# Performance work log

Hardware: AMD Instinct MI355X
Metric: run time of the kernel (lower is better)

The kernel has to match this reference:

```python
import jax, jax.numpy as jnp
import numpy as np

N = 50000      # num nodes
E = 800000     # num edges
D = 128        # num_hid
EPS = 1e-8


def _mlp(x, w1, b1, w2, b2):
    # 2-layer MLP: Linear -> ReLU -> Linear (dropout disabled at inference)
    return jax.nn.relu(x @ w1 + b1) @ w2 + b2


def setup_inputs() -> dict:
    key = jax.random.key(0)
    ks = jax.random.split(key, 12)

    def lin(k, fan_in, fan_out):
        kw, kb = jax.random.split(k)
        lim = 1.0 / np.sqrt(fan_in)
        w = jax.random.uniform(kw, (fan_in, fan_out), jnp.float32, -lim, lim)
        b = jax.random.uniform(kb, (fan_out,), jnp.float32, -lim, lim)
        return w, b

    H = jax.random.normal(ks[0], (N, D), jnp.float32)
    edge_index = jax.random.randint(ks[1], (2, E), 0, N, jnp.int64)
    w1_1, b1_1 = lin(ks[2], 2 * D, D)   # mlp_1 layer 1
    w1_2, b1_2 = lin(ks[3], D, D)       # mlp_1 layer 2
    w2_1, b2_1 = lin(ks[4], 2 * D, D)   # mlp_2 layer 1
    w2_2, b2_2 = lin(ks[5], D, 1)       # mlp_2 layer 2 (channel_curv=False -> out=1)
    t = jnp.zeros((), jnp.float32)
    return {"t": t, "H": H, "edge_index": edge_index,
            "w1_1": w1_1, "b1_1": b1_1, "w1_2": w1_2, "b1_2": b1_2,
            "w2_1": w2_1, "b2_1": b2_1, "w2_2": w2_2, "b2_2": b2_2}


def reference(t, H, edge_index, w1_1, b1_1, w1_2, b1_2, w2_1, b2_1, w2_2, b2_2):
    src, dst = edge_index[0], edge_index[1]

    # damping: row-normalize H
    H = H / (jnp.linalg.norm(H, axis=1, keepdims=True) + EPS)

    H_i = H[src]                                    # [E, D]
    H_j = H[dst]                                    # [E, D]

    # curvature(H_i, H_j)
    c = jnp.concatenate((H_i, H_j), axis=1)         # [E, 2D]
    c = jax.nn.relu(_mlp(c, w1_1, b1_1, w1_2, b1_2))  # [E, D]
    c = jax.ops.segment_sum(c, src, num_segments=N)   # scatter-sum -> [N, D]
    c = jnp.concatenate((c[src], c[dst]), axis=1)     # [E, 2D]
    curv = _mlp(c, w2_1, b2_1, w2_2, b2_2)            # [E, 1]

    # damped edge message
    cos = jnp.sum(H_i * H_j, axis=1, keepdims=True)   # [E, 1]
    H_edge = curv * (H_j - cos * H_i)                 # [E, D]

    # scatter-mean over source node
    s = jax.ops.segment_sum(H_edge, src, num_segments=N)               # [N, D]
    cnt = jax.ops.segment_sum(jnp.ones((E, 1), H.dtype), src, num_segments=N)
    Hm = s / jnp.maximum(cnt, 1.0)

    # damping: row-normalize output
    return Hm / (jnp.linalg.norm(Hm, axis=1, keepdims=True) + EPS)
```

## Files before the change

kernel.cpp:

```cpp
#include <hip/hip_runtime.h>
#include <hip/hip_bf16.h>

#define D 128
#define EPS 1e-8f
#define E1S 136

typedef __attribute__((ext_vector_type(8))) short short8;
typedef __attribute__((ext_vector_type(4))) float f32x4;
typedef unsigned int uint;

__device__ inline short f2bf(float x) {
    union { float f; unsigned u; } v; v.f = x;
    unsigned u = v.u + 0x7fffu + ((v.u >> 16) & 1u);
    return (short)(u >> 16);
}
__device__ inline float b2f(short s) {
    union { unsigned u; float f; } v;
    v.u = ((unsigned)(unsigned short)s) << 16;
    return v.f;
}
__device__ inline float uasf(uint u) {
    union { unsigned u; float f; } v; v.u = u; return v.f;
}

__global__ void k_normalize(const float* __restrict__ H, short* __restrict__ Hnb, int N) {
    int row = blockIdx.x * 4 + (threadIdx.x >> 6);
    int lane = threadIdx.x & 63;
    if (row >= N) return;
    float2 v = reinterpret_cast<const float2*>(H + (size_t)row * D)[lane];
    float ss = v.x * v.x + v.y * v.y;
    #pragma unroll
    for (int off = 32; off; off >>= 1) ss += __shfl_xor(ss, off, 64);
    float scale = 1.0f / (sqrtf(ss) + EPS);
    uint p = ((uint)(unsigned short)f2bf(v.x * scale)) |
             (((uint)(unsigned short)f2bf(v.y * scale)) << 16);
    reinterpret_cast<uint*>(Hnb + (size_t)row * D)[lane] = p;
}

__global__ void k_hist(const int* __restrict__ src, int* __restrict__ deg, int E) {
    for (int e = blockIdx.x * blockDim.x + threadIdx.x; e < E; e += gridDim.x * blockDim.x)
        atomicAdd(&deg[src[e]], 1);
}

__global__ void k_scan(const int* __restrict__ deg, int* __restrict__ rowptr, int N) {
    __shared__ int wsum[16];
    __shared__ int carry;
    int t = threadIdx.x, lane = t & 63, w = t >> 6;
    if (t == 0) carry = 0;
    __syncthreads();
    for (int base = 0; base < N; base += 4096) {
        int i0 = base + t * 4;
        int a = 0, b = 0, c = 0, d = 0;
        if (i0 + 3 < N) {
            int4 v4 = *reinterpret_cast<const int4*>(deg + i0);
            a = v4.x; b = v4.y; c = v4.z; d = v4.w;
        } else {
            if (i0 < N) a = deg[i0];
            if (i0 + 1 < N) b = deg[i0 + 1];
            if (i0 + 2 < N) c = deg[i0 + 2];
            if (i0 + 3 < N) d = deg[i0 + 3];
        }
        int s1 = a + b, s2 = s1 + c, s3 = s2 + d;
        int v = s3;
        #pragma unroll
        for (int off = 1; off < 64; off <<= 1) {
            int u = __shfl_up(v, off, 64);
            if (lane >= off) v += u;
        }
        if (lane == 63) wsum[w] = v;
        __syncthreads();
        if (w == 0 && lane < 16) {
            int s = wsum[lane];
            #pragma unroll
            for (int off = 1; off < 16; off <<= 1) {
                int u = __shfl_up(s, off, 64);
                if (lane >= off) s += u;
            }
            wsum[lane] = s;
        }
        __syncthreads();
        int add = (w > 0 ? wsum[w - 1] : 0) + carry;
        int incl = v + add;
        int pre = incl - s3;
        if (i0 < N)     rowptr[i0 + 1] = pre + a;
        if (i0 + 1 < N) rowptr[i0 + 2] = pre + s1;
        if (i0 + 2 < N) rowptr[i0 + 3] = pre + s2;
        if (i0 + 3 < N) rowptr[i0 + 4] = pre + s3;
        __syncthreads();
        if (t == 1023) carry = incl;
        __syncthreads();
    }
    if (t == 0) rowptr[0] = 0;
}

__global__ void k_scatter(const int* __restrict__ src, const int* __restrict__ dst,
                          const int* __restrict__ rowptr, int* __restrict__ fill,
                          int* __restrict__ srcS, int* __restrict__ dstS, int E) {
    for (int e = blockIdx.x * blockDim.x + threadIdx.x; e < E; e += gridDim.x * blockDim.x) {
        int s = src[e];
        int pos = atomicAdd(&fill[s], 1);
        int idx = rowptr[s] + pos;
        srcS[idx] = s;
        dstS[idx] = dst[e];
    }
}

__global__ void k_prep_all(const float* __restrict__ w1_1, const float* __restrict__ w1_2,
                           const float* __restrict__ w2_1, short* __restrict__ Wt) {
    int b = blockIdx.x;
    int m = b >> 6;
    int idx = (b & 63) * 256 + threadIdx.x;
    int k = idx >> 7, n = idx & 127;
    const float* W = (m == 0) ? w1_1
                   : (m == 1) ? w1_1 + 16384
                   : (m == 2) ? w1_2
                   : (m == 3) ? w2_1
                              : w2_1 + 16384;
    Wt[m * 16384 + n * 128 + k] = f2bf(W[k * 128 + n]);
}

template <bool A_BF16>
__global__ __launch_bounds__(256, 4)
void k_gemm_dual(const void* __restrict__ Aptr, const short* __restrict__ Wt0,
                 const short* __restrict__ Wt1, const float* __restrict__ bias0,
                 short* __restrict__ out0, short* __restrict__ out1, int N) {
    __shared__ short As[64 * E1S];
    int t = threadIdx.x;
    int r0 = blockIdx.x * 64;
    int l = t & 63, w = t >> 6, n0 = w * 32;
    {
        int er = t >> 2, kb = (t & 3) * 32;
        int rc = min(r0 + er, N - 1);
        if (A_BF16) {
            const short8* Ap = reinterpret_cast<const short8*>((const short*)Aptr + (size_t)rc * 128 + kb);
            #pragma unroll
            for (int q = 0; q < 4; ++q)
                *reinterpret_cast<short8*>(&As[er * E1S + kb + q * 8]) = Ap[q];
        } else {
            const float4* Ap = reinterpret_cast<const float4*>((const float*)Aptr + (size_t)rc * 128 + kb);
            #pragma unroll
            for (int q = 0; q < 4; ++q) {
                float4 a0 = Ap[q * 2], a1 = Ap[q * 2 + 1];
                short8 sv;
                sv[0] = f2bf(a0.x); sv[1] = f2bf(a0.y); sv[2] = f2bf(a0.z); sv[3] = f2bf(a0.w);
                sv[4] = f2bf(a1.x); sv[5] = f2bf(a1.y); sv[6] = f2bf(a1.z); sv[7] = f2bf(a1.w);
                *reinterpret_cast<short8*>(&As[er * E1S + kb + q * 8]) = sv;
            }
        }
    }
    short8 bfrag[2][4];
    #pragma unroll
    for (int nt = 0; nt < 2; ++nt) {
        int col = n0 + nt * 16 + (l & 15);
        #pragma unroll
        for (int kt = 0; kt < 4; ++kt)
            bfrag[nt][kt] = *reinterpret_cast<const short8*>(Wt0 + col * 128 + kt * 32 + (l >> 4) * 8);
    }
    float b0a = bias0[n0 + (l & 15)];
    float b0b = bias0[n0 + 16 + (l & 15)];
    __syncthreads();
    f32x4 acc0[4][2], acc1[4][2];
    #pragma unroll
    for (int mt = 0; mt < 4; ++mt) {
        acc0[mt][0] = (f32x4){0,0,0,0}; acc0[mt][1] = (f32x4){0,0,0,0};
        acc1[mt][0] = (f32x4){0,0,0,0}; acc1[mt][1] = (f32x4){0,0,0,0};
    }
    #pragma unroll
    for (int mt = 0; mt < 4; ++mt) {
        int arow = mt * 16 + (l & 15);
        #pragma unroll
        for (int kt = 0; kt < 4; ++kt) {
            short8 af = *reinterpret_cast<const short8*>(&As[arow * E1S + kt * 32 + (l >> 4) * 8]);
            acc0[mt][0] = __builtin_amdgcn_mfma_f32_16x16x32_bf16(af, bfrag[0][kt], acc0[mt][0], 0, 0, 0);
            acc0[mt][1] = __builtin_amdgcn_mfma_f32_16x16x32_bf16(af, bfrag[1][kt], acc0[mt][1], 0, 0, 0);
        }
    }
    #pragma unroll
    for (int nt = 0; nt < 2; ++nt) {
        int col = n0 + nt * 16 + (l & 15);
        #pragma unroll
        for (int kt = 0; kt < 4; ++kt)
            bfrag[nt][kt] = *reinterpret_cast<const short8*>(Wt1 + col * 128 + kt * 32 + (l >> 4) * 8);
    }
    #pragma unroll
    for (int mt = 0; mt < 4; ++mt) {
        int arow = mt * 16 + (l & 15);
        #pragma unroll
        for (int kt = 0; kt < 4; ++kt) {
            short8 af = *reinterpret_cast<const short8*>(&As[arow * E1S + kt * 32 + (l >> 4) * 8]);
            acc1[mt][0] = __builtin_amdgcn_mfma_f32_16x16x32_bf16(af, bfrag[0][kt], acc1[mt][0], 0, 0, 0);
            acc1[mt][1] = __builtin_amdgcn_mfma_f32_16x16x32_bf16(af, bfrag[1][kt], acc1[mt][1], 0, 0, 0);
        }
    }
    __syncthreads();
    #pragma unroll
    for (int mt = 0; mt < 4; ++mt)
        #pragma unroll
        for (int j = 0; j < 4; ++j) {
            int row = mt * 16 + (l >> 4) * 4 + j;
            As[row * E1S + n0 + (l & 15)]      = f2bf(acc0[mt][0][j] + b0a);
            As[row * E1S + n0 + 16 + (l & 15)] = f2bf(acc0[mt][1][j] + b0b);
        }
    __syncthreads();
    {
        int er = t >> 2, kb = (t & 3) * 32;
        int row = r0 + er;
        if (row < N)
            #pragma unroll
            for (int q = 0; q < 4; ++q)
                *reinterpret_cast<short8*>(out0 + (size_t)row * 128 + kb + q * 8) =
                    *reinterpret_cast<const short8*>(&As[er * E1S + kb + q * 8]);
    }
    __syncthreads();
    #pragma unroll
    for (int mt = 0; mt < 4; ++mt)
        #pragma unroll
        for (int j = 0; j < 4; ++j) {
            int row = mt * 16 + (l >> 4) * 4 + j;
            As[row * E1S + n0 + (l & 15)]      = f2bf(acc1[mt][0][j]);
            As[row * E1S + n0 + 16 + (l & 15)] = f2bf(acc1[mt][1][j]);
        }
    __syncthreads();
    {
        int er = t >> 2, kb = (t & 3) * 32;
        int row = r0 + er;
        if (row < N)
            #pragma unroll
            for (int q = 0; q < 4; ++q)
                *reinterpret_cast<short8*>(out1 + (size_t)row * 128 + kb + q * 8) =
                    *reinterpret_cast<const short8*>(&As[er * E1S + kb + q * 8]);
    }
}

__global__ __launch_bounds__(256, 5)
void k_edge_mlp1(const int* __restrict__ srcS, const int* __restrict__ dstS,
                 const int* __restrict__ rowptr,
                 const short* __restrict__ P, const short* __restrict__ Q,
                 const short* __restrict__ Wt, const float* __restrict__ b1_2,
                 float* __restrict__ C, int E) {
    __shared__ short e1s[64 * E1S];
    int t = threadIdx.x;
    int e0 = blockIdx.x * 64;
    int l = t & 63, w = t >> 6, n0 = w * 32;
    {
        int er = t >> 2, kb = (t & 3) * 32;
        int ge = min(e0 + er, E - 1);
        int sc = srcS[ge], dj = dstS[ge];
        const short8* Pp = reinterpret_cast<const short8*>(P + (size_t)sc * 128 + kb);
        const short8* Qp = reinterpret_cast<const short8*>(Q + (size_t)dj * 128 + kb);
        #pragma unroll
        for (int q = 0; q < 4; ++q) {
            short8 pv = Pp[q], qv = Qp[q];
            short8 sv;
            #pragma unroll
            for (int i = 0; i < 8; ++i)
                sv[i] = f2bf(fmaxf(b2f(pv[i]) + b2f(qv[i]), 0.f));
            *reinterpret_cast<short8*>(&e1s[er * E1S + kb + q * 8]) = sv;
        }
    }
    short8 bfrag[2][4];
    #pragma unroll
    for (int nt = 0; nt < 2; ++nt) {
        int col = n0 + nt * 16 + (l & 15);
        #pragma unroll
        for (int kt = 0; kt < 4; ++kt)
            bfrag[nt][kt] = *reinterpret_cast<const short8*>(Wt + col * 128 + kt * 32 + (l >> 4) * 8);
    }
    float bias0 = b1_2[n0 + (l & 15)];
    float bias1 = b1_2[n0 + 16 + (l & 15)];
    __syncthreads();
    f32x4 acc[4][2];
    #pragma unroll
    for (int mt = 0; mt < 4; ++mt) { acc[mt][0] = (f32x4){0,0,0,0}; acc[mt][1] = (f32x4){0,0,0,0}; }
    #pragma unroll
    for (int mt = 0; mt < 4; ++mt) {
        int arow = mt * 16 + (l & 15);
        #pragma unroll
        for (int kt = 0; kt < 4; ++kt) {
            short8 af = *reinterpret_cast<const short8*>(&e1s[arow * E1S + kt * 32 + (l >> 4) * 8]);
            acc[mt][0] = __builtin_amdgcn_mfma_f32_16x16x32_bf16(af, bfrag[0][kt], acc[mt][0], 0, 0, 0);
            acc[mt][1] = __builtin_amdgcn_mfma_f32_16x16x32_bf16(af, bfrag[1][kt], acc[mt][1], 0, 0, 0);
        }
    }
    #pragma unroll
    for (int mt = 0; mt < 4; ++mt)
        #pragma unroll
        for (int j = 0; j < 4; ++j) {
            acc[mt][0][j] = fmaxf(acc[mt][0][j] + bias0, 0.f);
            acc[mt][1][j] = fmaxf(acc[mt][1][j] + bias1, 0.f);
        }
    int myv = (e0 + l < E) ? srcS[e0 + l] : -1;
    int pv = __shfl_up(myv, 1, 64);
    bool head = (l == 0) || (myv != pv);
    unsigned long long validm = __ballot(myv >= 0);
    unsigned long long hm = __ballot(head) & validm;
    int nvalid = __popcll(validm);
    int grp = l >> 4;
    while (hm) {
        int lo = __builtin_ctzll(hm);
        hm &= hm - 1;
        int hi = hm ? __builtin_ctzll(hm) : nvalid;
        int s = __shfl(myv, lo, 64);
        float v0 = 0.f, v1 = 0.f;
        #pragma unroll
        for (int mt = 0; mt < 4; ++mt)
            #pragma unroll
            for (int j = 0; j < 4; ++j) {
                int row = mt * 16 + grp * 4 + j;
                bool in = (row >= lo) && (row < hi);
                v0 += in ? acc[mt][0][j] : 0.f;
                v1 += in ? acc[mt][1][j] : 0.f;
            }
        v0 += __shfl_xor(v0, 16, 64); v0 += __shfl_xor(v0, 32, 64);
        v1 += __shfl_xor(v1, 16, 64); v1 += __shfl_xor(v1, 32, 64);
        if (l < 16) {
            int rs = rowptr[s], re = rowptr[s + 1];
            float* cp = C + (size_t)s * 128 + n0 + l;
            if (rs >= e0 && re <= e0 + 64) {
                cp[0] = v0; cp[16] = v1;
            } else {
                atomicAdd(cp, v0); atomicAdd(cp + 16, v1);
            }
        }
    }
}

__global__ void k_edge_scal(const int* __restrict__ srcS, const int* __restrict__ dstS,
                            const short* __restrict__ Hnb,
                            const short* __restrict__ Rb, const short* __restrict__ Tb,
                            const float* __restrict__ w2_2, const float* __restrict__ b2_2,
                            float2* __restrict__ CC, int E) {
    int t = threadIdx.x;
    int e = blockIdx.x * 16 + (t >> 4);
    int sl = t & 15;
    if (e >= E) return;
    int s = srcS[e], d = dstS[e];
    uint4 hiu = reinterpret_cast<const uint4*>(Hnb + (size_t)s * 128)[sl];
    uint4 hju = reinterpret_cast<const uint4*>(Hnb + (size_t)d * 128)[sl];
    uint4 rvu = reinterpret_cast<const uint4*>(Rb + (size_t)s * 128)[sl];
    uint4 tvu = reinterpret_cast<const uint4*>(Tb + (size_t)d * 128)[sl];
    float4 wv0 = reinterpret_cast<const float4*>(w2_2)[sl * 2];
    float4 wv1 = reinterpret_cast<const float4*>(w2_2)[sl * 2 + 1];
    const float* wvp = &wv0.x;
    float pcos = 0.f, pcur = 0.f;
    const uint* hip = &hiu.x;
    const uint* hjp = &hju.x;
    const uint* rvp = &rvu.x;
    const uint* tvp = &tvu.x;
    #pragma unroll
    for (int k = 0; k < 4; ++k) {
        float hix = uasf(hip[k] << 16), hiy = uasf(hip[k] & 0xffff0000u);
        float hjx = uasf(hjp[k] << 16), hjy = uasf(hjp[k] & 0xffff0000u);
        float rvx = uasf(rvp[k] << 16), rvy = uasf(rvp[k] & 0xffff0000u);
        float tvx = uasf(tvp[k] << 16), tvy = uasf(tvp[k] & 0xffff0000u);
        float w0 = (k < 2) ? ((k == 0) ? wv0.x : wv0.z) : ((k == 2) ? wv1.x : wv1.z);
        float w1 = (k < 2) ? ((k == 0) ? wv0.y : wv0.w) : ((k == 2) ? wv1.y : wv1.w);
        pcos += hix * hjx + hiy * hjy;
        pcur += fmaxf(rvx + tvx, 0.f) * w0 + fmaxf(rvy + tvy, 0.f) * w1;
    }
    (void)wvp;
    #pragma unroll
    for (int off = 1; off < 16; off <<= 1) {
        pcos += __shfl_xor(pcos, off, 64);
        pcur += __shfl_xor(pcur, off, 64);
    }
    if (sl == 0)
        CC[e] = make_float2(pcur + b2_2[0], pcos);
}

__global__ void k_node_curv(const int* __restrict__ dstS, const int* __restrict__ rowptr,
                            const short* __restrict__ Hnb, const float2* __restrict__ CC,
                            float* __restrict__ out, int N) {
    int node = blockIdx.x * 4 + (threadIdx.x >> 6);
    int lane = threadIdx.x & 63;
    if (node >= N) return;
    uint hiu = reinterpret_cast<const uint*>(Hnb + (size_t)node * 128)[lane];
    float hix = uasf(hiu << 16), hiy = uasf(hiu & 0xffff0000u);
    int lo = rowptr[node], hiE = rowptr[node + 1];
    float ax = 0.f, ay = 0.f, sc = 0.f;
    for (int e = lo; e < hiE; ++e) {
        int d = dstS[e];
        float2 cc = CC[e];
        uint hju = reinterpret_cast<const uint*>(Hnb + (size_t)d * 128)[lane];
        float hjx = uasf(hju << 16), hjy = uasf(hju & 0xffff0000u);
        ax += cc.x * hjx;
        ay += cc.x * hjy;
        sc += cc.x * cc.y;
    }
    float inv = 1.0f / fmaxf((float)(hiE - lo), 1.0f);
    ax = (ax - sc * hix) * inv;
    ay = (ay - sc * hiy) * inv;
    float ss = ax * ax + ay * ay;
    #pragma unroll
    for (int off = 32; off; off >>= 1) ss += __shfl_xor(ss, off, 64);
    float scale = 1.0f / (sqrtf(ss) + EPS);
    reinterpret_cast<float2*>(out + (size_t)node * 128)[lane] = make_float2(ax * scale, ay * scale);
}

extern "C" void kernel_launch(void* const* d_in, const int* in_sizes, int n_in,
                              void* d_out, int out_size, void* d_ws, size_t ws_size,
                              hipStream_t stream) {
    const float* H    = (const float*)d_in[1];
    const int*   ei   = (const int*)d_in[2];
    const float* w1_1 = (const float*)d_in[3];
    const float* b1_1 = (const float*)d_in[4];
    const float* w1_2 = (const float*)d_in[5];
    const float* b1_2 = (const float*)d_in[6];
    const float* w2_1 = (const float*)d_in[7];
    const float* b2_1 = (const float*)d_in[8];
    const float* w2_2 = (const float*)d_in[9];
    const float* b2_2 = (const float*)d_in[10];

    int N = in_sizes[1] / D;
    int E = in_sizes[2] / 2;
    const int* src = ei;
    const int* dst = ei + E;

    float* out = (float*)d_out;

    short* Hnb  = (short*)d_ws;
    short* Pb   = Hnb + (size_t)N * D;
    short* Qb   = Pb + (size_t)N * D;
    float* Cb   = (float*)(Qb + (size_t)N * D);
    float2* CC  = (float2*)(Cb + (size_t)N * D);
    short* Wt   = (short*)(CC + E);
    int* deg    = (int*)(Wt + 5 * 16384);
    int* rowptr = deg + N;
    int* fill   = rowptr + N + 1;
    int* srcS   = fill + N;
    int* dstS   = srcS + E;

    hipMemsetAsync(Cb, 0, (size_t)N * D * sizeof(float), stream);
    hipMemsetAsync(deg, 0, (3 * (size_t)N + 1) * sizeof(int), stream);

    k_normalize<<<(N + 3) / 4, 256, 0, stream>>>(H, Hnb, N);
    k_hist<<<1024, 256, 0, stream>>>(src, deg, E);
    k_scan<<<1, 1024, 0, stream>>>(deg, rowptr, N);
    k_scatter<<<1024, 256, 0, stream>>>(src, dst, rowptr, fill, srcS, dstS, E);
    k_prep_all<<<320, 256, 0, stream>>>(w1_1, w1_2, w2_1, Wt);

    k_gemm_dual<true><<<(N + 63) / 64, 256, 0, stream>>>(Hnb, Wt + 0 * 16384, Wt + 1 * 16384,
                                                         b1_1, Pb, Qb, N);
    k_edge_mlp1<<<(E + 63) / 64, 256, 0, stream>>>(srcS, dstS, rowptr, Pb, Qb,
                                                   Wt + 2 * 16384, b1_2, Cb, E);
    k_gemm_dual<false><<<(N + 63) / 64, 256, 0, stream>>>(Cb, Wt + 3 * 16384, Wt + 4 * 16384,
                                                          b2_1, Pb, Qb, N);
    k_edge_scal<<<(E + 15) / 16, 256, 0, stream>>>(srcS, dstS, Hnb, Pb, Qb, w2_2, b2_2, CC, E);
    k_node_curv<<<(N + 3) / 4, 256, 0, stream>>>(dstS, rowptr, Hnb, CC, out, N);
}
```

Baseline: 412.0 us.

## Switch intermediates to fp16 and fuse edge scalar kernel into node aggregation

Replaces bf16 storage and MFMA with fp16 throughout, which simplifies conversions and lets the edge_mlp1 relu-add be done with packed half arithmetic. It also removes the separate per-edge scalar kernel and its CC buffer, computing curvature and cosine inside the per-node CSR loop with full-wave reductions. This saves a launch and the E-sized intermediate round trip, and the source-side R row is loaded once per node. In exchange, each edge iteration in the node loop now runs two 6-step shuffle reductions serially, and fp16 has a narrower range than bf16.

Result: slower. 425.2 us (+3.2%).

```diff
diff --git a/kernel.cpp b/kernel.cpp
--- a/kernel.cpp
+++ b/kernel.cpp
@@ -5,25 +5,23 @@
 #define EPS 1e-8f
 #define E1S 136
 
-typedef __attribute__((ext_vector_type(8))) short short8;
+typedef _Float16 f16;
+typedef __attribute__((ext_vector_type(8))) _Float16 half8;
 typedef __attribute__((ext_vector_type(4))) float f32x4;
 typedef unsigned int uint;
 
-__device__ inline short f2bf(float x) {
-    union { float f; unsigned u; } v; v.f = x;
-    unsigned u = v.u + 0x7fffu + ((v.u >> 16) & 1u);
-    return (short)(u >> 16);
-}
-__device__ inline float b2f(short s) {
-    union { unsigned u; float f; } v;
-    v.u = ((unsigned)(unsigned short)s) << 16;
-    return v.f;
-}
-__device__ inline float uasf(uint u) {
-    union { unsigned u; float f; } v; v.u = u; return v.f;
-}
-
-__global__ void k_normalize(const float* __restrict__ H, short* __restrict__ Hnb, int N) {
+__device__ inline short f2h(float x) {
+    union { f16 h; short s; } v; v.h = (f16)x; return v.s;
+}
+__device__ inline float h2f(short s) {
+    union { short s; f16 h; } v; v.s = s; return (float)v.h;
+}
+__device__ inline float2 up2(uint u) {
+    union { uint u; f16 h[2]; } v; v.u = u;
+    return make_float2((float)v.h[0], (float)v.h[1]);
+}
+
+__global__ void k_normalize(const float* __restrict__ H, f16* __restrict__ Hn, int N) {
     int row = blockIdx.x * 4 + (threadIdx.x >> 6);
     int lane = threadIdx.x & 63;
     if (row >= N) return;
@@ -32,9 +30,10 @@
     #pragma unroll
     for (int off = 32; off; off >>= 1) ss += __shfl_xor(ss, off, 64);
     float scale = 1.0f / (sqrtf(ss) + EPS);
-    uint p = ((uint)(unsigned short)f2bf(v.x * scale)) |
-             (((uint)(unsigned short)f2bf(v.y * scale)) << 16);
-    reinterpret_cast<uint*>(Hnb + (size_t)row * D)[lane] = p;
+    union { f16 h[2]; uint u; } p;
+    p.h[0] = (f16)(v.x * scale);
+    p.h[1] = (f16)(v.y * scale);
+    reinterpret_cast<uint*>(Hn + (size_t)row * D)[lane] = p.u;
 }
 
 __global__ void k_hist(const int* __restrict__ src, int* __restrict__ deg, int E) {
@@ -106,7 +105,7 @@
 }
 
 __global__ void k_prep_all(const float* __restrict__ w1_1, const float* __restrict__ w1_2,
-                           const float* __restrict__ w2_1, short* __restrict__ Wt) {
+                           const float* __restrict__ w2_1, f16* __restrict__ Wt) {
     int b = blockIdx.x;
     int m = b >> 6;
     int idx = (b & 63) * 256 + threadIdx.x;
@@ -116,45 +115,45 @@
                    : (m == 2) ? w1_2
                    : (m == 3) ? w2_1
                               : w2_1 + 16384;
-    Wt[m * 16384 + n * 128 + k] = f2bf(W[k * 128 + n]);
-}
-
-template <bool A_BF16>
+    Wt[m * 16384 + n * 128 + k] = (f16)W[k * 128 + n];
+}
+
+template <bool A_F16>
 __global__ __launch_bounds__(256, 4)
-void k_gemm_dual(const void* __restrict__ Aptr, const short* __restrict__ Wt0,
-                 const short* __restrict__ Wt1, const float* __restrict__ bias0,
-                 short* __restrict__ out0, short* __restrict__ out1, int N) {
-    __shared__ short As[64 * E1S];
+void k_gemm_dual(const void* __restrict__ Aptr, const f16* __restrict__ Wt0,
+                 const f16* __restrict__ Wt1, const float* __restrict__ bias0,
+                 f16* __restrict__ out0, f16* __restrict__ out1, int N) {
+    __shared__ f16 As[64 * E1S];
     int t = threadIdx.x;
     int r0 = blockIdx.x * 64;
     int l = t & 63, w = t >> 6, n0 = w * 32;
     {
         int er = t >> 2, kb = (t & 3) * 32;
         int rc = min(r0 + er, N - 1);
-        if (A_BF16) {
-            const short8* Ap = reinterpret_cast<const short8*>((const short*)Aptr + (size_t)rc * 128 + kb);
+        if (A_F16) {
+            const half8* Ap = reinterpret_cast<const half8*>((const f16*)Aptr + (size_t)rc * 128 + kb);
             #pragma unroll
             for (int q = 0; q < 4; ++q)
-                *reinterpret_cast<short8*>(&As[er * E1S + kb + q * 8]) = Ap[q];
+                *reinterpret_cast<half8*>(&As[er * E1S + kb + q * 8]) = Ap[q];
         } else {
             const float4* Ap = reinterpret_cast<const float4*>((const float*)Aptr + (size_t)rc * 128 + kb);
             #pragma unroll
             for (int q = 0; q < 4; ++q) {
                 float4 a0 = Ap[q * 2], a1 = Ap[q * 2 + 1];
-                short8 sv;
-                sv[0] = f2bf(a0.x); sv[1] = f2bf(a0.y); sv[2] = f2bf(a0.z); sv[3] = f2bf(a0.w);
-                sv[4] = f2bf(a1.x); sv[5] = f2bf(a1.y); sv[6] = f2bf(a1.z); sv[7] = f2bf(a1.w);
-                *reinterpret_cast<short8*>(&As[er * E1S + kb + q * 8]) = sv;
+                half8 sv;
+                sv[0] = (f16)a0.x; sv[1] = (f16)a0.y; sv[2] = (f16)a0.z; sv[3] = (f16)a0.w;
+                sv[4] = (f16)a1.x; sv[5] = (f16)a1.y; sv[6] = (f16)a1.z; sv[7] = (f16)a1.w;
+                *reinterpret_cast<half8*>(&As[er * E1S + kb + q * 8]) = sv;
             }
         }
     }
-    short8 bfrag[2][4];
+    half8 bfrag[2][4];
     #pragma unroll
     for (int nt = 0; nt < 2; ++nt) {
         int col = n0 + nt * 16 + (l & 15);
         #pragma unroll
         for (int kt = 0; kt < 4; ++kt)
-            bfrag[nt][kt] = *reinterpret_cast<const short8*>(Wt0 + col * 128 + kt * 32 + (l >> 4) * 8);
+            bfrag[nt][kt] = *reinterpret_cast<const half8*>(Wt0 + col * 128 + kt * 32 + (l >> 4) * 8);
     }
     float b0a = bias0[n0 + (l & 15)];
     float b0b = bias0[n0 + 16 + (l & 15)];
@@ -170,9 +169,9 @@
         int arow = mt * 16 + (l & 15);
         #pragma unroll
         for (int kt = 0; kt < 4; ++kt) {
-            short8 af = *reinterpret_cast<const short8*>(&As[arow * E1S + kt * 32 + (l >> 4) * 8]);
-            acc0[mt][0] = __builtin_amdgcn_mfma_f32_16x16x32_bf16(af, bfrag[0][kt], acc0[mt][0], 0, 0, 0);
-            acc0[mt][1] = __builtin_amdgcn_mfma_f32_16x16x32_bf16(af, bfrag[1][kt], acc0[mt][1], 0, 0, 0);
+            half8 af = *reinterpret_cast<const half8*>(&As[arow * E1S + kt * 32 + (l >> 4) * 8]);
+            acc0[mt][0] = __builtin_amdgcn_mfma_f32_16x16x32_f16(af, bfrag[0][kt], acc0[mt][0], 0, 0, 0);
+            acc0[mt][1] = __builtin_amdgcn_mfma_f32_16x16x32_f16(af, bfrag[1][kt], acc0[mt][1], 0, 0, 0);
         }
     }
     #pragma unroll
@@ -180,16 +179,16 @@
         int col = n0 + nt * 16 + (l & 15);
         #pragma unroll
         for (int kt = 0; kt < 4; ++kt)
-            bfrag[nt][kt] = *reinterpret_cast<const short8*>(Wt1 + col * 128 + kt * 32 + (l >> 4) * 8);
+            bfrag[nt][kt] = *reinterpret_cast<const half8*>(Wt1 + col * 128 + kt * 32 + (l >> 4) * 8);
     }
     #pragma unroll
     for (int mt = 0; mt < 4; ++mt) {
         int arow = mt * 16 + (l & 15);
         #pragma unroll
         for (int kt = 0; kt < 4; ++kt) {
-            short8 af = *reinterpret_cast<const short8*>(&As[arow * E1S + kt * 32 + (l >> 4) * 8]);
-            acc1[mt][0] = __builtin_amdgcn_mfma_f32_16x16x32_bf16(af, bfrag[0][kt], acc1[mt][0], 0, 0, 0);
-            acc1[mt][1] = __builtin_amdgcn_mfma_f32_16x16x32_bf16(af, bfrag[1][kt], acc1[mt][1], 0, 0, 0);
+            half8 af = *reinterpret_cast<const half8*>(&As[arow * E1S + kt * 32 + (l >> 4) * 8]);
+            acc1[mt][0] = __builtin_amdgcn_mfma_f32_16x16x32_f16(af, bfrag[0][kt], acc1[mt][0], 0, 0, 0);
+            acc1[mt][1] = __builtin_amdgcn_mfma_f32_16x16x32_f16(af, bfrag[1][kt], acc1[mt][1], 0, 0, 0);
         }
     }
     __syncthreads();
@@ -198,8 +197,8 @@
         #pragma unroll
         for (int j = 0; j < 4; ++j) {
             int row = mt * 16 + (l >> 4) * 4 + j;
-            As[row * E1S + n0 + (l & 15)]      = f2bf(acc0[mt][0][j] + b0a);
-            As[row * E1S + n0 + 16 + (l & 15)] = f2bf(acc0[mt][1][j] + b0b);
+            As[row * E1S + n0 + (l & 15)]      = (f16)(acc0[mt][0][j] + b0a);
+            As[row * E1S + n0 + 16 + (l & 15)] = (f16)(acc0[mt][1][j] + b0b);
         }
     __syncthreads();
     {
@@ -208,8 +207,8 @@
         if (row < N)
             #pragma unroll
             for (int q = 0; q < 4; ++q)
-                *reinterpret_cast<short8*>(out0 + (size_t)row * 128 + kb + q * 8) =
-                    *reinterpret_cast<const short8*>(&As[er * E1S + kb + q * 8]);
+                *reinterpret_cast<half8*>(out0 + (size_t)row * 128 + kb + q * 8) =
+                    *reinterpret_cast<const half8*>(&As[er * E1S + kb + q * 8]);
     }
     __syncthreads();
     #pragma unroll
@@ -217,8 +216,8 @@
         #pragma unroll
         for (int j = 0; j < 4; ++j) {
             int row = mt * 16 + (l >> 4) * 4 + j;
-            As[row * E1S + n0 + (l & 15)]      = f2bf(acc1[mt][0][j]);
-            As[row * E1S + n0 + 16 + (l & 15)] = f2bf(acc1[mt][1][j]);
+            As[row * E1S + n0 + (l & 15)]      = (f16)acc1[mt][0][j];
+            As[row * E1S + n0 + 16 + (l & 15)] = (f16)acc1[mt][1][j];
         }
     __syncthreads();
     {
@@ -227,18 +226,18 @@
         if (row < N)
             #pragma unroll
             for (int q = 0; q < 4; ++q)
-                *reinterpret_cast<short8*>(out1 + (size_t)row * 128 + kb + q * 8) =
-                    *reinterpret_cast<const short8*>(&As[er * E1S + kb + q * 8]);
+                *reinterpret_cast<half8*>(out1 + (size_t)row * 128 + kb + q * 8) =
+                    *reinterpret_cast<const half8*>(&As[er * E1S + kb + q * 8]);
     }
 }
 
 __global__ __launch_bounds__(256, 5)
 void k_edge_mlp1(const int* __restrict__ srcS, const int* __restrict__ dstS,
                  const int* __restrict__ rowptr,
-                 const short* __restrict__ P, const short* __restrict__ Q,
-                 const short* __restrict__ Wt, const float* __restrict__ b1_2,
+                 const f16* __restrict__ P, const f16* __restrict__ Q,
+                 const f16* __restrict__ Wt, const float* __restrict__ b1_2,
                  float* __restrict__ C, int E) {
-    __shared__ short e1s[64 * E1S];
+    __shared__ f16 e1s[64 * E1S];
     int t = threadIdx.x;
     int e0 = blockIdx.x * 64;
     int l = t & 63, w = t >> 6, n0 = w * 32;
@@ -246,25 +245,24 @@
         int er = t >> 2, kb = (t & 3) * 32;
         int ge = min(e0 + er, E - 1);
         int sc = srcS[ge], dj = dstS[ge];
-        const short8* Pp = reinterpret_cast<const short8*>(P + (size_t)sc * 128 + kb);
-        const short8* Qp = reinterpret_cast<const short8*>(Q + (size_t)dj * 128 + kb);
+        const half8* Pp = reinterpret_cast<const half8*>(P + (size_t)sc * 128 + kb);
+        const half8* Qp = reinterpret_cast<const half8*>(Q + (size_t)dj * 128 + kb);
         #pragma unroll
         for (int q = 0; q < 4; ++q) {
-            short8 pv = Pp[q], qv = Qp[q];
-            short8 sv;
+            half8 sv = Pp[q] + Qp[q];
             #pragma unroll
             for (int i = 0; i < 8; ++i)
-                sv[i] = f2bf(fmaxf(b2f(pv[i]) + b2f(qv[i]), 0.f));
-            *reinterpret_cast<short8*>(&e1s[er * E1S + kb + q * 8]) = sv;
-        }
-    }
-    short8 bfrag[2][4];
+                sv[i] = sv[i] > (f16)0 ? sv[i] : (f16)0;
+            *reinterpret_cast<half8*>(&e1s[er * E1S + kb + q * 8]) = sv;
+        }
+    }
+    half8 bfrag[2][4];
     #pragma unroll
     for (int nt = 0; nt < 2; ++nt) {
         int col = n0 + nt * 16 + (l & 15);
         #pragma unroll
         for (int kt = 0; kt < 4; ++kt)
-            bfrag[nt][kt] = *reinterpret_cast<const short8*>(Wt + col * 128 + kt * 32 + (l >> 4) * 8);
+            bfrag[nt][kt] = *reinterpret_cast<const half8*>(Wt + col * 128 + kt * 32 + (l >> 4) * 8);
     }
     float bias0 = b1_2[n0 + (l & 15)];
     float bias1 = b1_2[n0 + 16 + (l & 15)];
@@ -277,9 +275,9 @@
         int arow = mt * 16 + (l & 15);
         #pragma unroll
         for (int kt = 0; kt < 4; ++kt) {
-            short8 af = *reinterpret_cast<const short8*>(&e1s[arow * E1S + kt * 32 + (l >> 4) * 8]);
-            acc[mt][0] = __builtin_amdgcn_mfma_f32_16x16x32_bf16(af, bfrag[0][kt], acc[mt][0], 0, 0, 0);
-            acc[mt][1] = __builtin_amdgcn_mfma_f32_16x16x32_bf16(af, bfrag[1][kt], acc[mt][1], 0, 0, 0);
+            half8 af = *reinterpret_cast<const half8*>(&e1s[arow * E1S + kt * 32 + (l >> 4) * 8]);
+            acc[mt][0] = __builtin_amdgcn_mfma_f32_16x16x32_f16(af, bfrag[0][kt], acc[mt][0], 0, 0, 0);
+            acc[mt][1] = __builtin_amdgcn_mfma_f32_16x16x32_f16(af, bfrag[1][kt], acc[mt][1], 0, 0, 0);
         }
     }
     #pragma unroll
@@ -325,71 +323,39 @@
     }
 }
 
-__global__ void k_edge_scal(const int* __restrict__ srcS, const int* __restrict__ dstS,
-                            const short* __restrict__ Hnb,
-                            const short* __restrict__ Rb, const short* __restrict__ Tb,
+__global__ void k_node_curv(const int* __restrict__ dstS, const int* __restrict__ rowptr,
+                            const f16* __restrict__ Hn,
+                            const f16* __restrict__ Rb, const f16* __restrict__ Tb,
                             const float* __restrict__ w2_2, const float* __restrict__ b2_2,
-                            float2* __restrict__ CC, int E) {
-    int t = threadIdx.x;
-    int e = blockIdx.x * 16 + (t >> 4);
-    int sl = t & 15;
-    if (e >= E) return;
-    int s = srcS[e], d = dstS[e];
-    uint4 hiu = reinterpret_cast<const uint4*>(Hnb + (size_t)s * 128)[sl];
-    uint4 hju = reinterpret_cast<const uint4*>(Hnb + (size_t)d * 128)[sl];
-    uint4 rvu = reinterpret_cast<const uint4*>(Rb + (size_t)s * 128)[sl];
-    uint4 tvu = reinterpret_cast<const uint4*>(Tb + (size_t)d * 128)[sl];
-    float4 wv0 = reinterpret_cast<const float4*>(w2_2)[sl * 2];
-    float4 wv1 = reinterpret_cast<const float4*>(w2_2)[sl * 2 + 1];
-    const float* wvp = &wv0.x;
-    float pcos = 0.f, pcur = 0.f;
-    const uint* hip = &hiu.x;
-    const uint* hjp = &hju.x;
-    const uint* rvp = &rvu.x;
-    const uint* tvp = &tvu.x;
-    #pragma unroll
-    for (int k = 0; k < 4; ++k) {
-        float hix = uasf(hip[k] << 16), hiy = uasf(hip[k] & 0xffff0000u);
-        float hjx = uasf(hjp[k] << 16), hjy = uasf(hjp[k] & 0xffff0000u);
-        float rvx = uasf(rvp[k] << 16), rvy = uasf(rvp[k] & 0xffff0000u);
-        float tvx = uasf(tvp[k] << 16), tvy = uasf(tvp[k] & 0xffff0000u);
-        float w0 = (k < 2) ? ((k == 0) ? wv0.x : wv0.z) : ((k == 2) ? wv1.x : wv1.z);
-        float w1 = (k < 2) ? ((k == 0) ? wv0.y : wv0.w) : ((k == 2) ? wv1.y : wv1.w);
-        pcos += hix * hjx + hiy * hjy;
-        pcur += fmaxf(rvx + tvx, 0.f) * w0 + fmaxf(rvy + tvy, 0.f) * w1;
-    }
-    (void)wvp;
-    #pragma unroll
-    for (int off = 1; off < 16; off <<= 1) {
-        pcos += __shfl_xor(pcos, off, 64);
-        pcur += __shfl_xor(pcur, off, 64);
-    }
-    if (sl == 0)
-        CC[e] = make_float2(pcur + b2_2[0], pcos);
-}
-
-__global__ void k_node_curv(const int* __restrict__ dstS, const int* __restrict__ rowptr,
-                            const short* __restrict__ Hnb, const float2* __restrict__ CC,
                             float* __restrict__ out, int N) {
     int node = blockIdx.x * 4 + (threadIdx.x >> 6);
     int lane = threadIdx.x & 63;
     if (node >= N) return;
-    uint hiu = reinterpret_cast<const uint*>(Hnb + (size_t)node * 128)[lane];
-    float hix = uasf(hiu << 16), hiy = uasf(hiu & 0xffff0000u);
+    float2 hi = up2(reinterpret_cast<const uint*>(Hn + (size_t)node * 128)[lane]);
+    float2 rv = up2(reinterpret_cast<const uint*>(Rb + (size_t)node * 128)[lane]);
+    float2 wv = reinterpret_cast<const float2*>(w2_2)[lane];
+    float bb = b2_2[0];
     int lo = rowptr[node], hiE = rowptr[node + 1];
     float ax = 0.f, ay = 0.f, sc = 0.f;
     for (int e = lo; e < hiE; ++e) {
         int d = dstS[e];
-        float2 cc = CC[e];
-        uint hju = reinterpret_cast<const uint*>(Hnb + (size_t)d * 128)[lane];
-        float hjx = uasf(hju << 16), hjy = uasf(hju & 0xffff0000u);
-        ax += cc.x * hjx;
-        ay += cc.x * hjy;
-        sc += cc.x * cc.y;
+        float2 hj = up2(reinterpret_cast<const uint*>(Hn + (size_t)d * 128)[lane]);
+        float2 tv = up2(reinterpret_cast<const uint*>(Tb + (size_t)d * 128)[lane]);
+        float pcos = hi.x * hj.x + hi.y * hj.y;
+        float pcur = fmaxf(rv.x + tv.x, 0.f) * wv.x + fmaxf(rv.y + tv.y, 0.f) * wv.y;
+        #pragma unroll
+        for (int off = 1; off < 64; off <<= 1) {
+            pcos += __shfl_xor(pcos, off, 64);
+            pcur += __shfl_xor(pcur, off, 64);
+        }
+        float cur = pcur + bb;
+        ax += cur * hj.x;
+        ay += cur * hj.y;
+        sc += cur * pcos;
     }
     float inv = 1.0f / fmaxf((float)(hiE - lo), 1.0f);
-    ax = (ax - sc * hix) * inv;
-    ay = (ay - sc * hiy) * inv;
+    ax = (ax - sc * hi.x) * inv;
+    ay = (ay - sc * hi.y) * inv;
     float ss = ax * ax + ay * ay;
     #pragma unroll
     for (int off = 32; off; off >>= 1) ss += __shfl_xor(ss, off, 64);
@@ -418,12 +384,11 @@
 
     float* out = (float*)d_out;
 
-    short* Hnb  = (short*)d_ws;
-    short* Pb   = Hnb + (size_t)N * D;
-    short* Qb   = Pb + (size_t)N * D;
+    f16* Hnb    = (f16*)d_ws;
+    f16* Pb     = Hnb + (size_t)N * D;
+    f16* Qb     = Pb + (size_t)N * D;
     float* Cb   = (float*)(Qb + (size_t)N * D);
-    float2* CC  = (float2*)(Cb + (size_t)N * D);
-    short* Wt   = (short*)(CC + E);
+    f16* Wt     = (f16*)(Cb + (size_t)N * D);
     int* deg    = (int*)(Wt + 5 * 16384);
     int* rowptr = deg + N;
     int* fill   = rowptr + N + 1;
@@ -445,6 +410,5 @@
                                                    Wt + 2 * 16384, b1_2, Cb, E);
     k_gemm_dual<false><<<(N + 63) / 64, 256, 0, stream>>>(Cb, Wt + 3 * 16384, Wt + 4 * 16384,
                                                           b2_1, Pb, Qb, N);
-    k_edge_scal<<<(E + 15) / 16, 256, 0, stream>>>(srcS, dstS, Hnb, Pb, Qb, w2_2, b2_2, CC, E);
-    k_node_curv<<<(N + 3) / 4, 256, 0, stream>>>(dstS, rowptr, Hnb, CC, out, N);
-}
+    k_node_curv<<<(N + 3) / 4, 256, 0, stream>>>(dstS, rowptr, Hnb, Pb, Qb, w2_2, b2_2, out, N);
+}
```
